# Optimization experiments

Measured on AMD Instinct MI355X. Metric: run time of the kernel, lower is better.

Reference implementation:

```python
import jax, jax.numpy as jnp
import numpy as np

N = 100000
H1, D1 = 8, 8          # conv1: 8 heads x 8 dims (concat -> 64)
C = 40                 # num_classes, conv2: 1 head
NEG_SLOPE = 0.2


def gat_layer(x, edge_index, W, a_src, a_dst, b, heads, out_dim, concat):
    # x: [N, F_in], W: [F_in, heads*out_dim], a_*: [heads, out_dim], b: [heads*out_dim] or [out_dim]
    h = (x @ W).reshape(-1, heads, out_dim)                 # [N, H, D]
    s_src = jnp.einsum('nhd,hd->nh', h, a_src)              # [N, H]
    s_dst = jnp.einsum('nhd,hd->nh', h, a_dst)              # [N, H]
    src, dst = edge_index[0], edge_index[1]
    e = jax.nn.leaky_relu(s_src[src] + s_dst[dst], NEG_SLOPE)   # [E, H]
    # segment softmax over incoming edges of each dst node
    m = jax.ops.segment_max(e, dst, num_segments=N)         # [N, H]
    e = jnp.exp(e - m[dst])
    z = jax.ops.segment_sum(e, dst, num_segments=N)         # [N, H]
    alpha = e / (z[dst] + 1e-16)                            # [E, H]
    msg = h[src] * alpha[:, :, None]                        # [E, H, D]
    out = jax.ops.segment_sum(msg, dst, num_segments=N)     # [N, H, D]
    if concat:
        out = out.reshape(-1, heads * out_dim)
    else:
        out = out.mean(axis=1)
    return out + b


def setup_inputs() -> dict:
    key = jax.random.key(0)
    ks = jax.random.split(key, 10)
    F_in = 256
    x = jax.random.normal(ks[0], (N, F_in), dtype=jnp.float32)
    edge_index = jax.random.randint(ks[1], (2, 1600000), 0, N, dtype=jnp.int32)
    sc1 = 1.0 / np.sqrt(F_in)
    W1 = jax.random.normal(ks[2], (F_in, H1 * D1), dtype=jnp.float32) * sc1
    a1_src = jax.random.normal(ks[3], (H1, D1), dtype=jnp.float32) * 0.1
    a1_dst = jax.random.normal(ks[4], (H1, D1), dtype=jnp.float32) * 0.1
    b1 = jnp.zeros((H1 * D1,), dtype=jnp.float32)
    sc2 = 1.0 / np.sqrt(H1 * D1)
    W2 = jax.random.normal(ks[5], (H1 * D1, C), dtype=jnp.float32) * sc2
    a2_src = jax.random.normal(ks[6], (1, C), dtype=jnp.float32) * 0.1
    a2_dst = jax.random.normal(ks[7], (1, C), dtype=jnp.float32) * 0.1
    b2 = jnp.zeros((C,), dtype=jnp.float32)
    return {"x": x, "edge_index": edge_index, "W1": W1, "a1_src": a1_src,
            "a1_dst": a1_dst, "b1": b1, "W2": W2, "a2_src": a2_src,
            "a2_dst": a2_dst, "b2": b2}


def reference(x, edge_index, W1, a1_src, a1_dst, b1, W2, a2_src, a2_dst, b2):
    # eval mode: dropout is identity
    h = gat_layer(x, edge_index, W1, a1_src, a1_dst, b1, H1, D1, concat=True)
    h = jax.nn.elu(h)
    out = gat_layer(h, edge_index, W2, a2_src, a2_dst, b2, 1, C, concat=False)
    return jax.nn.log_softmax(out, axis=1)
```

## Files before the change

kernel.cpp:

```cpp
#include <hip/hip_runtime.h>
#include <math.h>

#define BK 10
#define KNODES 1024
#define MAXNB 128

typedef __attribute__((ext_vector_type(8))) short bf16x8;
typedef __attribute__((ext_vector_type(4))) float f32x4;

__device__ __forceinline__ float bf2f(unsigned short u) {
  return __uint_as_float(((unsigned int)u) << 16);
}
__device__ __forceinline__ unsigned short f2bf(float f) {
  unsigned int i = __float_as_uint(f);
  unsigned int r = i + 0x7FFFu + ((i >> 16) & 1u);
  return (unsigned short)(r >> 16);
}

__global__ __launch_bounds__(256) void prep_kernel(
    const float* __restrict__ W1, const float* __restrict__ W2,
    const float* __restrict__ a2s, const float* __restrict__ a2d,
    unsigned short* __restrict__ whi, unsigned short* __restrict__ wlo,
    unsigned short* __restrict__ w2hi, unsigned short* __restrict__ w2lo,
    float* __restrict__ vas, float* __restrict__ vad,
    unsigned short* __restrict__ h1b, unsigned short* __restrict__ h2b,
    float* __restrict__ s1s, float* __restrict__ s2s,
    int* __restrict__ bpos, int capP, int NN) {
  const int blk = blockIdx.x, t = threadIdx.x;
  if (blk == 0 && t < MAXNB) bpos[t] = t * capP;
  if (blk < 32) {
    if (t < 64) {
      int b = blk, lane = t;
      int kt = b >> 2, ct = b & 3;
      int n = lane & 15, g = lane >> 4;
      unsigned short hb[8], lb[8];
#pragma unroll
      for (int j = 0; j < 8; ++j) {
        int k = kt * 32 + g * 8 + j;
        float wv = W1[k * 64 + ct * 16 + n];
        unsigned short hi = f2bf(wv);
        float rem = wv - bf2f(hi);
        hb[j] = hi;
        lb[j] = f2bf(rem);
      }
      size_t base = ((size_t)b * 64 + lane) * 8;
      *(ushort4*)(whi + base)     = make_ushort4(hb[0], hb[1], hb[2], hb[3]);
      *(ushort4*)(whi + base + 4) = make_ushort4(hb[4], hb[5], hb[6], hb[7]);
      *(ushort4*)(wlo + base)     = make_ushort4(lb[0], lb[1], lb[2], lb[3]);
      *(ushort4*)(wlo + base + 4) = make_ushort4(lb[4], lb[5], lb[6], lb[7]);
    }
  } else if (blk == 32) {
    if (t < 64) {
      float s = 0.f, d = 0.f;
      for (int c = 0; c < 40; ++c) {
        float w = W2[t * 40 + c];
        s += w * a2s[c];
        d += w * a2d[c];
      }
      vas[t] = s;
      vad[t] = d;
    }
  } else if (blk == 33) {
    if (t < 64) {
      h1b[(size_t)NN * 64 + t] = 0;
      if (t < 40) h2b[(size_t)NN * 40 + t] = 0;
      if (t < 8)  s1s[(size_t)NN * 8 + t] = -1e30f;
      if (t == 0) s2s[NN] = -1e30f;
    }
  } else if (blk >= 34 && blk < 40) {
    if (t < 64) {
      int b = blk - 34;
      int kt = b / 3, ct = b % 3;
      int n = t & 15, g = t >> 4;
      unsigned short hb[8], lb[8];
#pragma unroll
      for (int j = 0; j < 8; ++j) {
        int k = kt * 32 + g * 8 + j;
        int c = ct * 16 + n;
        float wv = (c < 40) ? W2[k * 40 + c] : 0.f;
        unsigned short hi = f2bf(wv);
        float rem = wv - bf2f(hi);
        hb[j] = hi;
        lb[j] = f2bf(rem);
      }
      size_t base = ((size_t)b * 64 + t) * 8;
      *(ushort4*)(w2hi + base)     = make_ushort4(hb[0], hb[1], hb[2], hb[3]);
      *(ushort4*)(w2hi + base + 4) = make_ushort4(hb[4], hb[5], hb[6], hb[7]);
      *(ushort4*)(w2lo + base)     = make_ushort4(lb[0], lb[1], lb[2], lb[3]);
      *(ushort4*)(w2lo + base + 4) = make_ushort4(lb[4], lb[5], lb[6], lb[7]);
    }
  }
}

__global__ __launch_bounds__(256) void gemm1_mfma_kernel(
    const float* __restrict__ x, const unsigned short* __restrict__ whi,
    const unsigned short* __restrict__ wlo,
    const float* __restrict__ a_src, const float* __restrict__ a_dst,
    unsigned short* __restrict__ h1b,
    float* __restrict__ s_src, float* __restrict__ s_dst, int N) {
  const int w = threadIdx.x >> 6, lane = threadIdx.x & 63;
  const int m = lane & 15, g = lane >> 4;
  const int rbase = blockIdx.x * 64 + w * 16;
  int arow = rbase + m;
  if (arow >= N) arow = N - 1;
  const float* xrow = x + (size_t)arow * 256 + g * 8;
  f32x4 acc[4] = {{0.f, 0.f, 0.f, 0.f}, {0.f, 0.f, 0.f, 0.f},
                  {0.f, 0.f, 0.f, 0.f}, {0.f, 0.f, 0.f, 0.f}};
#pragma unroll
  for (int kt = 0; kt < 8; ++kt) {
    float4 a0 = *(const float4*)(xrow + kt * 32);
    float4 a1 = *(const float4*)(xrow + kt * 32 + 4);
    float av[8] = {a0.x, a0.y, a0.z, a0.w, a1.x, a1.y, a1.z, a1.w};
    bf16x8 ahi, alo;
#pragma unroll
    for (int j = 0; j < 8; ++j) {
      unsigned int u = __float_as_uint(av[j]);
      unsigned short hi = (unsigned short)(u >> 16);
      float rem = av[j] - bf2f(hi);
      ahi[j] = (short)hi;
      alo[j] = (short)(__float_as_uint(rem) >> 16);
    }
    const unsigned short* wp = whi + ((size_t)(kt * 4) * 64 + lane) * 8;
    const unsigned short* lp = wlo + ((size_t)(kt * 4) * 64 + lane) * 8;
#pragma unroll
    for (int ct = 0; ct < 4; ++ct) {
      bf16x8 bh = *(const bf16x8*)(wp + (size_t)ct * 64 * 8);
      bf16x8 bl = *(const bf16x8*)(lp + (size_t)ct * 64 * 8);
      acc[ct] = __builtin_amdgcn_mfma_f32_16x16x32_bf16(ahi, bh, acc[ct], 0, 0, 0);
      acc[ct] = __builtin_amdgcn_mfma_f32_16x16x32_bf16(alo, bh, acc[ct], 0, 0, 0);
      acc[ct] = __builtin_amdgcn_mfma_f32_16x16x32_bf16(ahi, bl, acc[ct], 0, 0, 0);
    }
  }
#pragma unroll
  for (int r = 0; r < 4; ++r) {
    int ro = rbase + g * 4 + r;
    if (ro < N) {
#pragma unroll
      for (int ct = 0; ct < 4; ++ct)
        h1b[(size_t)ro * 64 + ct * 16 + m] = f2bf(acc[ct][r]);
    }
  }
  float a1sv[4], a1dv[4];
#pragma unroll
  for (int ct = 0; ct < 4; ++ct) {
    a1sv[ct] = a_src[ct * 16 + m];
    a1dv[ct] = a_dst[ct * 16 + m];
  }
#pragma unroll
  for (int r = 0; r < 4; ++r) {
    float ps[4], pd[4];
#pragma unroll
    for (int ct = 0; ct < 4; ++ct) {
      ps[ct] = acc[ct][r] * a1sv[ct];
      pd[ct] = acc[ct][r] * a1dv[ct];
    }
#pragma unroll
    for (int off = 1; off < 8; off <<= 1) {
#pragma unroll
      for (int ct = 0; ct < 4; ++ct) {
        ps[ct] += __shfl_xor(ps[ct], off);
        pd[ct] += __shfl_xor(pd[ct], off);
      }
    }
    int ro = rbase + g * 4 + r;
    if ((m & 7) == 0 && ro < N) {
      int hb2 = m >> 3;
#pragma unroll
      for (int ct = 0; ct < 4; ++ct) {
        s_src[(size_t)ro * 8 + ct * 2 + hb2] = ps[ct];
        s_dst[(size_t)ro * 8 + ct * 2 + hb2] = pd[ct];
      }
    }
  }
}

__global__ __launch_bounds__(256) void bin_kernel(const int* __restrict__ src,
                                                  const int* __restrict__ dst,
                                                  int* __restrict__ bpos,
                                                  unsigned int* __restrict__ payload,
                                                  int E, int NB, int capP) {
  __shared__ int hist[MAXNB], soff[MAXNB], base[MAXNB], rnk[MAXNB];
  __shared__ unsigned int stage[4096];
  const int t = threadIdx.x;
  const int e0 = blockIdx.x * 4096;
  if (t < MAXNB) { hist[t] = 0; rnk[t] = 0; }
  __syncthreads();
  for (int j = t; j < 4096; j += 256) {
    int e = e0 + j;
    if (e < E) atomicAdd(&hist[dst[e] >> BK], 1);
  }
  __syncthreads();
  if (t == 0) {
    int acc = 0;
    for (int b = 0; b < NB; ++b) { soff[b] = acc; acc += hist[b]; }
  }
  __syncthreads();
  if (t < NB) {
    int c = hist[t];
    base[t] = c ? atomicAdd(&bpos[t], c) : 0;
  }
  __syncthreads();
  for (int j = t; j < 4096; j += 256) {
    int e = e0 + j;
    if (e < E) {
      int d = dst[e];
      int b = d >> BK;
      int s = src[e];
      int r = atomicAdd(&rnk[b], 1);
      stage[soff[b] + r] = (((unsigned)(d & (KNODES - 1))) << 17) | (unsigned)s;
    }
  }
  __syncthreads();
  int wave = t >> 6, lane = t & 63;
  for (int b = wave; b < NB; b += 4) {
    int len = hist[b], bs = soff[b], gb = base[b];
    int lim = (b + 1) * capP;
    for (int j = lane; j < len; j += 64)
      if (gb + j < lim) payload[gb + j] = stage[bs + j];
  }
}

__global__ __launch_bounds__(1024) void fill2_kernel(const unsigned int* __restrict__ payload,
                                                     const int* __restrict__ bpos,
                                                     int* __restrict__ col,
                                                     int* __restrict__ rbeg,
                                                     int* __restrict__ rend,
                                                     int capP, int NN) {
  __shared__ int cnt[KNODES], scn[KNODES], pos[KNODES];
  const int b = blockIdx.x, t = threadIdx.x;
  cnt[t] = 0;
  __syncthreads();
  const int beg = b * capP;
  int len = bpos[b] - beg;
  if (len > capP) len = capP;
  for (int j = t; j < len; j += 1024) atomicAdd(&cnt[payload[beg + j] >> 17], 1);
  __syncthreads();
  const int myc = cnt[t];
  const int padc = (myc + 7) & ~7;
  scn[t] = padc;
  __syncthreads();
  for (int off = 1; off < 1024; off <<= 1) {
    int v = (t >= off) ? scn[t - off] : 0;
    __syncthreads();
    scn[t] += v;
    __syncthreads();
  }
  const int mystart = b * (capP + 8 * KNODES) + scn[t] - padc;
  const int n = (b << BK) + t;
  if (n < NN) { rbeg[n] = mystart; rend[n] = mystart + padc; }
  pos[t] = mystart;
  __syncthreads();
  for (int j = t; j < len; j += 1024) {
    unsigned int pay = payload[beg + j];
    int p = atomicAdd(&pos[pay >> 17], 1);
    col[p] = (int)(pay & 0x1FFFF);
  }
  __syncthreads();
  for (int j = mystart + myc; j < mystart + padc; ++j) col[j] = NN;
}

__global__ __launch_bounds__(256) void agg1_kernel(
    const int* __restrict__ rbeg, const int* __restrict__ rend,
    const int* __restrict__ col,
    const float* __restrict__ s_src, const float* __restrict__ s_dst,
    const unsigned short* __restrict__ h1b, const float* __restrict__ b1,
    const float* __restrict__ vas, const float* __restrict__ vad,
    unsigned short* __restrict__ helub, float* __restrict__ s2s,
    float* __restrict__ s2d, int N) {
  int wv = threadIdx.x >> 6;
  int l  = threadIdx.x & 63;
  int n  = blockIdx.x * 4 + wv;
  if (n >= N) return;
  const int q  = l >> 3;
  const int hh = l & 7;
  const float sdq = s_dst[n * 8 + hh];
  const int beg = __builtin_amdgcn_readfirstlane(rbeg[n]);
  const int end = __builtin_amdgcn_readfirstlane(rend[n]);
  float z = 0.f, acc = 0.f, acc2 = 0.f;
  int e = beg;
  if (((end - beg) >> 3) & 1) {
    int4 ia = *(const int4*)(col + e);
    int4 ib = *(const int4*)(col + e + 4);
    int myidx = col[e + q];
    float pv = s_src[(unsigned)myidx * 8u + (unsigned)hh];
    float tt = pv + sdq;
    tt = fmaxf(tt, 0.2f * tt);
    float w = __expf(tt);
    z += w;
    int idxs[8] = {ia.x, ia.y, ia.z, ia.w, ib.x, ib.y, ib.z, ib.w};
#pragma unroll
    for (int j = 0; j < 8; ++j) {
      float wj = __shfl(w, j * 8 + q, 64);
      unsigned short g = h1b[(unsigned)idxs[j] * 64u + (unsigned)l];
      acc = fmaf(wj, bf2f(g), acc);
    }
    e += 8;
  }
  for (; e < end; e += 16) {
    int4 ia = *(const int4*)(col + e);
    int4 ib = *(const int4*)(col + e + 4);
    int4 ic = *(const int4*)(col + e + 8);
    int4 id = *(const int4*)(col + e + 12);
    int my0 = col[e + q];
    int my1 = col[e + 8 + q];
    float pv0 = s_src[(unsigned)my0 * 8u + (unsigned)hh];
    float pv1 = s_src[(unsigned)my1 * 8u + (unsigned)hh];
    int idxs[16] = {ia.x, ia.y, ia.z, ia.w, ib.x, ib.y, ib.z, ib.w,
                    ic.x, ic.y, ic.z, ic.w, id.x, id.y, id.z, id.w};
    unsigned short gg[16];
#pragma unroll
    for (int j = 0; j < 16; ++j) gg[j] = h1b[(unsigned)idxs[j] * 64u + (unsigned)l];
    float t0 = pv0 + sdq; t0 = fmaxf(t0, 0.2f * t0); float w0 = __expf(t0);
    float t1 = pv1 + sdq; t1 = fmaxf(t1, 0.2f * t1); float w1 = __expf(t1);
    z += w0 + w1;
#pragma unroll
    for (int j = 0; j < 8; ++j) {
      float wj = __shfl(w0, j * 8 + q, 64);
      acc = fmaf(wj, bf2f(gg[j]), acc);
    }
#pragma unroll
    for (int j = 0; j < 8; ++j) {
      float wj = __shfl(w1, j * 8 + q, 64);
      acc2 = fmaf(wj, bf2f(gg[8 + j]), acc2);
    }
  }
  acc += acc2;
  z += __shfl_xor(z, 8); z += __shfl_xor(z, 16); z += __shfl_xor(z, 32);
  float zf = __shfl(z, 9 * q, 64);
  float v = acc / (zf + 1e-16f) + b1[l];
  v = v > 0.f ? v : (__expf(v) - 1.f);
  helub[(size_t)n * 64 + l] = f2bf(v);
  float ps = v * vas[l];
  float pd = v * vad[l];
  for (int off = 32; off > 0; off >>= 1) {
    ps += __shfl_xor(ps, off);
    pd += __shfl_xor(pd, off);
  }
  if (l == 0) { s2s[n] = ps; s2d[n] = pd; }
}

__global__ __launch_bounds__(256) void gemm2_mfma_kernel(
    const unsigned short* __restrict__ heb, const unsigned short* __restrict__ w2hi,
    const unsigned short* __restrict__ w2lo, unsigned short* __restrict__ h2b, int N) {
  const int w = threadIdx.x >> 6, lane = threadIdx.x & 63;
  const int m = lane & 15, g = lane >> 4;
  const int rbase = blockIdx.x * 64 + w * 16;
  int arow = rbase + m;
  if (arow >= N) arow = N - 1;
  const unsigned short* hrow = heb + (size_t)arow * 64 + g * 8;
  f32x4 acc[3] = {{0.f, 0.f, 0.f, 0.f}, {0.f, 0.f, 0.f, 0.f}, {0.f, 0.f, 0.f, 0.f}};
#pragma unroll
  for (int kt = 0; kt < 2; ++kt) {
    bf16x8 a = *(const bf16x8*)(hrow + kt * 32);
#pragma unroll
    for (int ct = 0; ct < 3; ++ct) {
      int b = kt * 3 + ct;
      bf16x8 bh = *(const bf16x8*)(w2hi + ((size_t)b * 64 + lane) * 8);
      bf16x8 bl = *(const bf16x8*)(w2lo + ((size_t)b * 64 + lane) * 8);
      acc[ct] = __builtin_amdgcn_mfma_f32_16x16x32_bf16(a, bh, acc[ct], 0, 0, 0);
      acc[ct] = __builtin_amdgcn_mfma_f32_16x16x32_bf16(a, bl, acc[ct], 0, 0, 0);
    }
  }
#pragma unroll
  for (int r = 0; r < 4; ++r) {
    int ro = rbase + g * 4 + r;
    if (ro < N) {
#pragma unroll
      for (int ct = 0; ct < 3; ++ct) {
        int c = ct * 16 + m;
        if (c < 40) h2b[(size_t)ro * 40 + c] = f2bf(acc[ct][r]);
      }
    }
  }
}

__global__ __launch_bounds__(256) void agg2_kernel(
    const int* __restrict__ rbeg, const int* __restrict__ rend,
    const int* __restrict__ col,
    const float* __restrict__ s2s, const float* __restrict__ s2d,
    const unsigned short* __restrict__ h2b, const float* __restrict__ b2,
    float* __restrict__ out, int N) {
  int wv = threadIdx.x >> 6;
  int l  = threadIdx.x & 63;
  int n  = blockIdx.x * 4 + wv;
  if (n >= N) return;
  const int q = l >> 3;
  const bool act = (l < 40);
  const unsigned lc = act ? (unsigned)l : 0u;
  const float sdv = s2d[n];
  const int beg = __builtin_amdgcn_readfirstlane(rbeg[n]);
  const int end = __builtin_amdgcn_readfirstlane(rend[n]);
  float z = 0.f, acc = 0.f, acc2 = 0.f;
  int e = beg;
  if (((end - beg) >> 3) & 1) {
    int4 ia = *(const int4*)(col + e);
    int4 ib = *(const int4*)(col + e + 4);
    int myidx = col[e + q];
    float pv = s2s[myidx];
    float tt = pv + sdv;
    tt = fmaxf(tt, 0.2f * tt);
    float w = __expf(tt);
    z += w;
    int idxs[8] = {ia.x, ia.y, ia.z, ia.w, ib.x, ib.y, ib.z, ib.w};
#pragma unroll
    for (int j = 0; j < 8; ++j) {
      float wj = __shfl(w, j * 8, 64);
      unsigned short g = h2b[(unsigned)idxs[j] * 40u + lc];
      acc = fmaf(wj, bf2f(g), acc);
    }
    e += 8;
  }
  for (; e < end; e += 16) {
    int4 ia = *(const int4*)(col + e);
    int4 ib = *(const int4*)(col + e + 4);
    int4 ic = *(const int4*)(col + e + 8);
    int4 id = *(const int4*)(col + e + 12);
    int my0 = col[e + q];
    int my1 = col[e + 8 + q];
    float pv0 = s2s[my0];
    float pv1 = s2s[my1];
    int idxs[16] = {ia.x, ia.y, ia.z, ia.w, ib.x, ib.y, ib.z, ib.w,
                    ic.x, ic.y, ic.z, ic.w, id.x, id.y, id.z, id.w};
    unsigned short gg[16];
#pragma unroll
    for (int j = 0; j < 16; ++j) gg[j] = h2b[(unsigned)idxs[j] * 40u + lc];
    float t0 = pv0 + sdv; t0 = fmaxf(t0, 0.2f * t0); float w0 = __expf(t0);
    float t1 = pv1 + sdv; t1 = fmaxf(t1, 0.2f * t1); float w1 = __expf(t1);
    z += w0 + w1;
#pragma unroll
    for (int j = 0; j < 8; ++j) {
      float wj = __shfl(w0, j * 8, 64);
      acc = fmaf(wj, bf2f(gg[j]), acc);
    }
#pragma unroll
    for (int j = 0; j < 8; ++j) {
      float wj = __shfl(w1, j * 8, 64);
      acc2 = fmaf(wj, bf2f(gg[8 + j]), acc2);
    }
  }
  acc += acc2;
  z += __shfl_xor(z, 8); z += __shfl_xor(z, 16); z += __shfl_xor(z, 32);
  float v = act ? (acc / (z + 1e-16f) + b2[l]) : -1e30f;
  float m = v;
  for (int off = 32; off > 0; off >>= 1) m = fmaxf(m, __shfl_xor(m, off));
  float ex = act ? __expf(v - m) : 0.f;
  float s = ex;
  for (int off = 32; off > 0; off >>= 1) s += __shfl_xor(s, off);
  if (act) out[(size_t)n * 40 + l] = v - m - logf(s);
}

extern "C" void kernel_launch(void* const* d_in, const int* in_sizes, int n_in,
                              void* d_out, int out_size, void* d_ws, size_t ws_size,
                              hipStream_t stream) {
  const float* x   = (const float*)d_in[0];
  const int*   ei  = (const int*)d_in[1];
  const float* W1  = (const float*)d_in[2];
  const float* a1s = (const float*)d_in[3];
  const float* a1d = (const float*)d_in[4];
  const float* b1  = (const float*)d_in[5];
  const float* W2  = (const float*)d_in[6];
  const float* a2s = (const float*)d_in[7];
  const float* a2d = (const float*)d_in[8];
  const float* b2  = (const float*)d_in[9];
  float* out = (float*)d_out;
  (void)n_in; (void)out_size; (void)ws_size;

  const int NN = in_sizes[0] / 256;
  const int E  = in_sizes[1] / 2;
  const int NB = (NN + KNODES - 1) >> BK;
  const int* esrc = ei;
  const int* edst = ei + E;

  int capP = (E + NB - 1) / NB;
  capP += capP / 4 + capP / 16 + 512;
  capP = (capP + 15) & ~15;

  char* p = (char*)d_ws;
  auto alloc = [&](size_t bytes) -> char* {
    char* q = p;
    p += (bytes + 255) & ~(size_t)255;
    return q;
  };
  unsigned short* h1b   = (unsigned short*)alloc((size_t)(NN + 1) * 64 * 2);
  unsigned short* helub = (unsigned short*)alloc((size_t)NN * 64 * 2);
  unsigned short* h2b   = (unsigned short*)alloc((size_t)(NN + 1) * 40 * 2);
  float* s1s  = (float*)alloc((size_t)(NN + 1) * 8 * 4);
  float* s1d  = (float*)alloc((size_t)NN * 8 * 4);
  float* s2s  = (float*)alloc((size_t)(NN + 1) * 4);
  float* s2d  = (float*)alloc((size_t)NN * 4);
  int*   rbeg = (int*)alloc((size_t)NN * 4);
  int*   rend = (int*)alloc((size_t)NN * 4);
  int*   bpos = (int*)alloc(MAXNB * 4);
  unsigned int* payload = (unsigned int*)alloc((size_t)NB * capP * 4);
  int*   col  = (int*)alloc((size_t)NB * (capP + 8 * KNODES) * 4);
  float* vas  = (float*)alloc(64 * 4);
  float* vad  = (float*)alloc(64 * 4);
  unsigned short* w1hi = (unsigned short*)alloc(32 * 64 * 8 * 2);
  unsigned short* w1lo = (unsigned short*)alloc(32 * 64 * 8 * 2);
  unsigned short* w2hi = (unsigned short*)alloc(6 * 64 * 8 * 2);
  unsigned short* w2lo = (unsigned short*)alloc(6 * 64 * 8 * 2);

  prep_kernel<<<40, 256, 0, stream>>>(W1, W2, a2s, a2d, w1hi, w1lo, w2hi, w2lo,
                                      vas, vad, h1b, h2b, s1s, s2s, bpos, capP, NN);
  bin_kernel<<<(E + 4095) / 4096, 256, 0, stream>>>(esrc, edst, bpos, payload, E, NB, capP);
  fill2_kernel<<<NB, 1024, 0, stream>>>(payload, bpos, col, rbeg, rend, capP, NN);
  gemm1_mfma_kernel<<<(NN + 63) / 64, 256, 0, stream>>>(x, w1hi, w1lo, a1s, a1d,
                                                        h1b, s1s, s1d, NN);
  agg1_kernel<<<(NN + 3) / 4, 256, 0, stream>>>(rbeg, rend, col, s1s, s1d, h1b, b1,
                                                vas, vad, helub, s2s, s2d, NN);
  gemm2_mfma_kernel<<<(NN + 63) / 64, 256, 0, stream>>>(helub, w2hi, w2lo, h2b, NN);
  agg2_kernel<<<(NN + 3) / 4, 256, 0, stream>>>(rbeg, rend, col, s2s, s2d, h2b, b2, out, NN);
}
```

Before: 358.6 us.

## Stage x tiles into LDS with async loads, prefetch weights, use wave-shuffle scan

The first-layer GEMM now copies the 16-row x tile of each wave into a swizzled LDS buffer with global_load_lds, issuing every load up front. It then waits on the vmcnt counter one k-step at a time, so the later loads overlap with MFMA work. Weight fragments for the next k-step are double-buffered in registers. Separately, the CSR fill kernel replaces its 10-step block-wide LDS prefix scan, which had two barriers per step, with a wave-level shuffle scan plus a small cross-wave scan. The hand-coded vmcnt counts depend on the exact number of outstanding loads and could break if the compiler reorders or merges memory operations.

```diff
diff --git a/kernel.cpp b/kernel.cpp
--- a/kernel.cpp
+++ b/kernel.cpp
@@ -98,18 +98,67 @@
     const float* __restrict__ a_src, const float* __restrict__ a_dst,
     unsigned short* __restrict__ h1b,
     float* __restrict__ s_src, float* __restrict__ s_dst, int N) {
+  __shared__ float xtile[4][4096];
   const int w = threadIdx.x >> 6, lane = threadIdx.x & 63;
   const int m = lane & 15, g = lane >> 4;
+  const int msw = m & 7;
   const int rbase = blockIdx.x * 64 + w * 16;
-  int arow = rbase + m;
-  if (arow >= N) arow = N - 1;
-  const float* xrow = x + (size_t)arow * 256 + g * 8;
+  float* xw = xtile[w];
+
+  const int lrow8 = lane >> 3;
+  const int lch   = lane & 7;
+  const int gch   = lch ^ lrow8;
+#pragma unroll
+  for (int kt = 0; kt < 8; ++kt) {
+#pragma unroll
+    for (int rh = 0; rh < 2; ++rh) {
+      int rl = rh * 8 + lrow8;
+      int row = rbase + rl;
+      if (row >= N) row = N - 1;
+      const float* src = x + (size_t)row * 256 + kt * 32 + (gch << 2);
+      __builtin_amdgcn_global_load_lds(
+          (const __attribute__((address_space(1))) unsigned int*)src,
+          (__attribute__((address_space(3))) unsigned int*)(xw + (kt * 16 + rh * 8) * 32),
+          16, 0, 0);
+    }
+  }
+
   f32x4 acc[4] = {{0.f, 0.f, 0.f, 0.f}, {0.f, 0.f, 0.f, 0.f},
                   {0.f, 0.f, 0.f, 0.f}, {0.f, 0.f, 0.f, 0.f}};
+
+  const unsigned short* wp0 = whi + (size_t)lane * 8;
+  const unsigned short* lp0 = wlo + (size_t)lane * 8;
+  bf16x8 bh[4], bl[4];
+#pragma unroll
+  for (int ct = 0; ct < 4; ++ct) {
+    bh[ct] = *(const bf16x8*)(wp0 + (size_t)ct * 512);
+    bl[ct] = *(const bf16x8*)(lp0 + (size_t)ct * 512);
+  }
+
 #pragma unroll
   for (int kt = 0; kt < 8; ++kt) {
-    float4 a0 = *(const float4*)(xrow + kt * 32);
-    float4 a1 = *(const float4*)(xrow + kt * 32 + 4);
+    bf16x8 nh[4], nl[4];
+    if (kt < 7) {
+#pragma unroll
+      for (int ct = 0; ct < 4; ++ct) {
+        nh[ct] = *(const bf16x8*)(wp0 + (size_t)((kt + 1) * 4 + ct) * 512);
+        nl[ct] = *(const bf16x8*)(lp0 + (size_t)((kt + 1) * 4 + ct) * 512);
+      }
+    }
+    switch (kt) {
+      case 0: asm volatile("s_waitcnt vmcnt(14)" ::: "memory"); break;
+      case 1: asm volatile("s_waitcnt vmcnt(12)" ::: "memory"); break;
+      case 2: asm volatile("s_waitcnt vmcnt(10)" ::: "memory"); break;
+      case 3: asm volatile("s_waitcnt vmcnt(8)"  ::: "memory"); break;
+      case 4: asm volatile("s_waitcnt vmcnt(6)"  ::: "memory"); break;
+      case 5: asm volatile("s_waitcnt vmcnt(4)"  ::: "memory"); break;
+      case 6: asm volatile("s_waitcnt vmcnt(2)"  ::: "memory"); break;
+      case 7: asm volatile("s_waitcnt vmcnt(0)"  ::: "memory"); break;
+    }
+    const float* p0 = xw + (kt * 16 + m) * 32 + (((g * 2)     ^ msw) << 2);
+    const float* p1 = xw + (kt * 16 + m) * 32 + (((g * 2 + 1) ^ msw) << 2);
+    float4 a0 = *(const float4*)p0;
+    float4 a1 = *(const float4*)p1;
     float av[8] = {a0.x, a0.y, a0.z, a0.w, a1.x, a1.y, a1.z, a1.w};
     bf16x8 ahi, alo;
 #pragma unroll
@@ -120,15 +169,15 @@
       ahi[j] = (short)hi;
       alo[j] = (short)(__float_as_uint(rem) >> 16);
     }
-    const unsigned short* wp = whi + ((size_t)(kt * 4) * 64 + lane) * 8;
-    const unsigned short* lp = wlo + ((size_t)(kt * 4) * 64 + lane) * 8;
 #pragma unroll
     for (int ct = 0; ct < 4; ++ct) {
-      bf16x8 bh = *(const bf16x8*)(wp + (size_t)ct * 64 * 8);
-      bf16x8 bl = *(const bf16x8*)(lp + (size_t)ct * 64 * 8);
-      acc[ct] = __builtin_amdgcn_mfma_f32_16x16x32_bf16(ahi, bh, acc[ct], 0, 0, 0);
-      acc[ct] = __builtin_amdgcn_mfma_f32_16x16x32_bf16(alo, bh, acc[ct], 0, 0, 0);
-      acc[ct] = __builtin_amdgcn_mfma_f32_16x16x32_bf16(ahi, bl, acc[ct], 0, 0, 0);
+      acc[ct] = __builtin_amdgcn_mfma_f32_16x16x32_bf16(ahi, bh[ct], acc[ct], 0, 0, 0);
+      acc[ct] = __builtin_amdgcn_mfma_f32_16x16x32_bf16(alo, bh[ct], acc[ct], 0, 0, 0);
+      acc[ct] = __builtin_amdgcn_mfma_f32_16x16x32_bf16(ahi, bl[ct], acc[ct], 0, 0, 0);
+    }
+    if (kt < 7) {
+#pragma unroll
+      for (int ct = 0; ct < 4; ++ct) { bh[ct] = nh[ct]; bl[ct] = nl[ct]; }
     }
   }
 #pragma unroll
@@ -226,7 +275,8 @@
                                                      int* __restrict__ rbeg,
                                                      int* __restrict__ rend,
                                                      int capP, int NN) {
-  __shared__ int cnt[KNODES], scn[KNODES], pos[KNODES];
+  __shared__ int cnt[KNODES], pos[KNODES];
+  __shared__ int wsum[16];
   const int b = blockIdx.x, t = threadIdx.x;
   cnt[t] = 0;
   __syncthreads();
@@ -237,15 +287,27 @@
   __syncthreads();
   const int myc = cnt[t];
   const int padc = (myc + 7) & ~7;
-  scn[t] = padc;
-  __syncthreads();
-  for (int off = 1; off < 1024; off <<= 1) {
-    int v = (t >= off) ? scn[t - off] : 0;
-    __syncthreads();
-    scn[t] += v;
-    __syncthreads();
-  }
-  const int mystart = b * (capP + 8 * KNODES) + scn[t] - padc;
+  const int lane = t & 63, wid = t >> 6;
+  int v = padc;
+#pragma unroll
+  for (int off = 1; off < 64; off <<= 1) {
+    int u = __shfl_up(v, off, 64);
+    if (lane >= off) v += u;
+  }
+  if (lane == 63) wsum[wid] = v;
+  __syncthreads();
+  if (t < 16) {
+    int sv = wsum[t];
+#pragma unroll
+    for (int off = 1; off < 16; off <<= 1) {
+      int u = __shfl_up(sv, off, 64);
+      if ((int)t >= off) sv += u;
+    }
+    wsum[t] = sv;
+  }
+  __syncthreads();
+  const int incl = v + (wid ? wsum[wid - 1] : 0);
+  const int mystart = b * (capP + 8 * KNODES) + incl - padc;
   const int n = (b << BK) + t;
   if (n < NN) { rbeg[n] = mystart; rend[n] = mystart + padc; }
   pos[t] = mystart;
```

Result: no change. 352.3 us (-1.8%).
